# Kernel optimization log

Hardware: AMD Instinct MI355X
Metric: run time of the kernel (lower is better)

## Reference

```python
import jax, jax.numpy as jnp
import numpy as np

B, H, W = 64, 512, 512
T = 100           # num_thresholds
R = 8             # defect regions per image (max label id)
BLOCK = 128       # defect regions are 128x128 blocks on a 4x4 grid
SAT = 1.0         # saturation_threshold (relative)


def setup_inputs() -> dict:
    key = jax.random.key(0)
    k1, _ = jax.random.split(key)
    preds = jax.random.uniform(k1, (B, H, W), dtype=jnp.float32)
    thresholds = jnp.linspace(0.0, 1.0, T).astype(jnp.float32)
    # Build a labeled GT mask: R disjoint 128x128 block regions per image,
    # labels 1..R (0 = background). This plays the role of measure.label(target).
    rng = np.random.default_rng(0)
    labels = np.zeros((B, H, W), dtype=np.int32)
    gb = H // BLOCK           # 4 blocks per side -> 16 candidate blocks
    nblocks = gb * gb
    for b in range(B):
        chosen = rng.permutation(nblocks)[:R]
        for rid, blk in enumerate(chosen, start=1):
            r, c = divmod(int(blk), gb)
            labels[b, r * BLOCK:(r + 1) * BLOCK, c * BLOCK:(c + 1) * BLOCK] = rid
    return {"preds": preds, "thresholds": thresholds, "labels": jnp.asarray(labels)}


def reference(preds, thresholds, labels):
    # preds: (B,H,W) float32 in [0,1); thresholds: (T,) sorted; labels: (B,H,W) int32, 0=bg.
    Bn, Hn, Wn = preds.shape
    Tn = thresholds.shape[0]
    flat_s = preds.reshape(-1)
    flat_l = labels.reshape(-1)
    # bucket[p] = number of thresholds <= score[p]; pixel passes thr[t] iff bucket > t.
    bucket = jnp.searchsorted(thresholds, flat_s, side='right')  # int in [0, T]
    # ---- background FP / TN per threshold (exact counts via histogram) ----
    bg = (flat_l == 0).astype(jnp.int32)
    bg_hist = jax.ops.segment_sum(bg, bucket, num_segments=Tn + 1)  # (T+1,)
    bg_total = bg_hist.sum()
    fp = (bg_total - jnp.cumsum(bg_hist)[:Tn]).astype(jnp.float32)  # fp[t] = #bg with score>=thr[t]
    tn = bg_total.astype(jnp.float32) - fp
    # ---- per-region TP per threshold (segmented histogram) ----
    bidx = jnp.repeat(jnp.arange(Bn), Hn * Wn)
    seg = bidx * R + (flat_l - 1)              # region id in [0, B*R)
    comb = seg * (Tn + 1) + bucket
    NSEG = Bn * R * (Tn + 1)
    comb = jnp.where(flat_l > 0, comb, NSEG)   # dump bg pixels in overflow slot
    hist = jax.ops.segment_sum(jnp.ones_like(bucket, dtype=jnp.int32), comb,
                               num_segments=NSEG + 1)[:NSEG].reshape(Bn, R, Tn + 1)
    area = hist.sum(-1)                                       # (B,R) defect areas
    tp = (area[..., None] - jnp.cumsum(hist, -1)[..., :Tn]).astype(jnp.float32)  # (B,R,T)
    sat = jnp.maximum(area.astype(jnp.float32) * SAT, 1.0)    # relative saturation
    valid = (area > 0).astype(jnp.float32)                    # guard empty regions
    spro = jnp.minimum(tp / sat[..., None], 1.0) * valid[..., None]
    spro_sum = spro.sum((0, 1))                               # (T,)
    n_def = jnp.maximum(valid.sum(), 1.0)
    mean_spro = spro_sum / n_def
    # ---- AUC over FPR (max_fpr = 1.0) ----
    denom = fp + tn
    fpr = jnp.where(denom > 0, fp / jnp.maximum(denom, 1.0), 0.0)
    order = jnp.argsort(fpr)
    x = fpr[order]
    y = mean_spro[order]
    auc = jnp.sum((x[1:] - x[:-1]) * (y[1:] + y[:-1]) * 0.5)  # trapezoid rule
    return auc
```

## Files before the change

### kernel.cpp

```cpp
#include <hip/hip_runtime.h>

#define B_N 64
#define H_N 512
#define W_N 512
#define T_N 100
#define TB  101
#define R_N 8
#define NLAB 9
#define CHUNKS 32
#define PIX_PER_IMG (H_N * W_N)
#define CPIX (PIX_PER_IMG / CHUNKS)

__global__ __launch_bounds__(256, 8) void hist_kernel(
    const float* __restrict__ preds, const int* __restrict__ labels,
    const float* __restrict__ thr,
    int* __restrict__ region_hist,
    int* __restrict__ bg_hist)
{
    __shared__ float s_thr[T_N];
    __shared__ int whist[4][NLAB * TB];

    const int tid  = threadIdx.x;
    const int wave = tid >> 6;

    for (int i = tid; i < 4 * NLAB * TB; i += 256) ((int*)whist)[i] = 0;
    if (tid < T_N) s_thr[tid] = thr[tid];
    __syncthreads();

    const int img   = blockIdx.x >> 5;
    const int chunk = blockIdx.x & (CHUNKS - 1);
    const long base = (long)img * PIX_PER_IMG + (long)chunk * CPIX;
    const float4* p4 = (const float4*)(preds + base);
    const int4*   l4 = (const int4*)(labels + base);
    int* __restrict__ myh = whist[wave];

#pragma unroll
    for (int g = 0; g < 2; ++g) {
        float4 pv[4];
        int4   lv[4];
#pragma unroll
        for (int u = 0; u < 4; ++u) {
            pv[u] = p4[(g * 4 + u) * 256 + tid];
            lv[u] = l4[(g * 4 + u) * 256 + tid];
        }
#pragma unroll
        for (int u = 0; u < 4; ++u) {
            float ps[4] = {pv[u].x, pv[u].y, pv[u].z, pv[u].w};
            int   ls[4] = {lv[u].x, lv[u].y, lv[u].z, lv[u].w};
#pragma unroll
            for (int j = 0; j < 4; ++j) {
                float s = ps[j];
                int k = (int)(s * (float)(T_N - 1)) + 1;
                k = max(0, min(T_N, k));
                while (k < T_N && s_thr[k] <= s) ++k;
                while (k > 0 && s_thr[k - 1] > s) --k;
                atomicAdd(&myh[ls[j] * TB + k], 1);
            }
        }
    }
    __syncthreads();

    for (int i = tid; i < NLAB * TB; i += 256) {
        int v = whist[0][i] + whist[1][i] + whist[2][i] + whist[3][i];
        if (v) {
            int lab = i / TB;
            int t   = i - lab * TB;
            if (lab == 0)
                atomicAdd(&bg_hist[img * TB + t], v);
            else
                atomicAdd(&region_hist[(img * R_N + (lab - 1)) * TB + t], v);
        }
    }
}

__global__ __launch_bounds__(128) void region_final_kernel(
    const int* __restrict__ region_hist,
    const int* __restrict__ bg_hist,
    float* __restrict__ spro_sum,
    int* __restrict__ n_def,
    int* __restrict__ bgh_total,
    int* __restrict__ done_ctr,
    float* __restrict__ out)
{
    __shared__ float spro_sh[R_N][T_N];
    __shared__ int validc[R_N];
    __shared__ int s_ticket;
    const int img = blockIdx.x;
    const int tid = threadIdx.x;

    if (tid < TB) atomicAdd(&bgh_total[tid], bg_hist[img * TB + tid]);

    if (tid < R_N) {
        const int* h = &region_hist[(img * R_N + tid) * TB];
        int area = 0;
        for (int t = 0; t < TB; ++t) area += h[t];
        float sat   = fmaxf((float)area, 1.0f);
        float valid = (area > 0) ? 1.0f : 0.0f;
        int csum = 0;
        for (int t = 0; t < T_N; ++t) {
            csum += h[t];
            float tp = (float)(area - csum);
            spro_sh[tid][t] = fminf(tp / sat, 1.0f) * valid;
        }
        validc[tid] = (area > 0) ? 1 : 0;
    }
    __syncthreads();

    if (tid < T_N) {
        float s = 0.0f;
        for (int r = 0; r < R_N; ++r) s += spro_sh[r][tid];
        atomicAdd(&spro_sum[tid], s);
    }
    if (tid == 0) {
        int v = 0;
        for (int r = 0; r < R_N; ++r) v += validc[r];
        atomicAdd(n_def, v);
    }

    __threadfence();
    if (tid == 0)
        s_ticket = __hip_atomic_fetch_add(done_ctr, 1, __ATOMIC_ACQ_REL,
                                          __HIP_MEMORY_SCOPE_AGENT);
    __syncthreads();
    if (s_ticket != B_N - 1) return;

    __shared__ int    bgh[TB];
    __shared__ float  s_spro[T_N];
    __shared__ float  fpr_sh[T_N];
    __shared__ float  ms_sh[T_N];
    __shared__ int    order[T_N];
    __shared__ double contrib[T_N];
    __shared__ int    s_nd;

    if (tid < TB)
        bgh[tid] = __hip_atomic_load(&bgh_total[tid], __ATOMIC_RELAXED,
                                     __HIP_MEMORY_SCOPE_AGENT);
    if (tid < T_N)
        s_spro[tid] = __hip_atomic_load(&spro_sum[tid], __ATOMIC_RELAXED,
                                        __HIP_MEMORY_SCOPE_AGENT);
    if (tid == 0)
        s_nd = __hip_atomic_load(n_def, __ATOMIC_RELAXED,
                                 __HIP_MEMORY_SCOPE_AGENT);
    __syncthreads();

    if (tid < T_N) {
        int fp_i = 0;
        for (int k = tid + 1; k < TB; ++k) fp_i += bgh[k];
        int tot = fp_i;
        for (int k = 0; k <= tid; ++k) tot += bgh[k];
        float bgt = (float)tot;
        float fp  = (float)fp_i;
        fpr_sh[tid] = (bgt > 0.0f) ? fp / fmaxf(bgt, 1.0f) : 0.0f;
        float nd = fmaxf((float)s_nd, 1.0f);
        ms_sh[tid] = s_spro[tid] / nd;
    }
    __syncthreads();

    if (tid < T_N) {
        float v = fpr_sh[tid];
        int r = 0;
        for (int j = 0; j < T_N; ++j) {
            float u = fpr_sh[j];
            r += (u < v) | ((u == v) & (j < tid));
        }
        order[r] = tid;
    }
    __syncthreads();

    if (tid < T_N - 1) {
        int o0 = order[tid], o1 = order[tid + 1];
        double x0 = fpr_sh[o0], x1 = fpr_sh[o1];
        double y0 = ms_sh[o0],  y1 = ms_sh[o1];
        contrib[tid] = (x1 - x0) * (y0 + y1) * 0.5;
    } else if (tid < T_N) {
        contrib[tid] = 0.0;
    }
    __syncthreads();

    if (tid == 0) {
        double s = 0.0;
        for (int i = 0; i < T_N - 1; ++i) s += contrib[i];
        out[0] = (float)s;
    }
}

extern "C" void kernel_launch(void* const* d_in, const int* in_sizes, int n_in,
                              void* d_out, int out_size, void* d_ws, size_t ws_size,
                              hipStream_t stream) {
    const float* preds  = (const float*)d_in[0];
    const float* thr    = (const float*)d_in[1];
    const int*   labels = (const int*)d_in[2];
    float* out = (float*)d_out;

    int*   region_hist = (int*)d_ws;
    int*   bg_hist     = region_hist + B_N * R_N * TB;
    int*   bgh_total   = bg_hist + B_N * TB;
    float* spro_sum    = (float*)(bgh_total + TB);
    int*   n_def       = (int*)(spro_sum + T_N);
    int*   done_ctr    = n_def + 1;

    size_t zbytes = sizeof(int) * (size_t)(B_N * R_N * TB + B_N * TB + TB)
                  + sizeof(float) * T_N + 2 * sizeof(int);
    hipMemsetAsync(d_ws, 0, zbytes, stream);

    hist_kernel<<<B_N * CHUNKS, 256, 0, stream>>>(preds, labels, thr,
                                                  region_hist, bg_hist);
    region_final_kernel<<<B_N, 128, 0, stream>>>(region_hist, bg_hist, spro_sum,
                                                 n_def, bgh_total, done_ctr, out);
}
```

Baseline: 172.5 us.

## Fuse histogram and finalize kernels; use LUT for threshold bucket lookup

Merges the per-region finalize and AUC stages into the histogram kernel using per-image and global completion counters, so the last chunk block of each image computes its sPRO and the last image block computes the AUC. This drops one kernel launch. It also replaces the linear threshold search with a 256-cell shared-memory lookup table plus a bounds check, falling back to the old search only when the check fails. Shared memory is reused through a union, and the extra fences and atomics add a serialized tail at the end.

New measurement: 542.9 us. 3.15x slower.

```diff
diff --git a/kernel.cpp b/kernel.cpp
--- a/kernel.cpp
+++ b/kernel.cpp
@@ -10,21 +10,59 @@
 #define CHUNKS 32
 #define PIX_PER_IMG (H_N * W_N)
 #define CPIX (PIX_PER_IMG / CHUNKS)
-
-__global__ __launch_bounds__(256, 8) void hist_kernel(
+#define NCELL 256
+
+struct LutE { float tlo, thrb, thi; int klo; };
+
+union TailU {
+    int whist[4][NLAB * TB];
+    struct {
+        double contrib[T_N];
+        int    rh[R_N * TB];
+        float  spro[R_N][T_N];
+        int    validc[R_N];
+        int    bgh[TB];
+        float  fpr[T_N];
+        float  ms[T_N];
+        int    order[T_N];
+        int    nd;
+    } t;
+};
+
+__global__ __launch_bounds__(256, 8) void fused_kernel(
     const float* __restrict__ preds, const int* __restrict__ labels,
     const float* __restrict__ thr,
     int* __restrict__ region_hist,
-    int* __restrict__ bg_hist)
+    int* __restrict__ bg_hist,
+    float* __restrict__ spro_sum,
+    int* __restrict__ n_def,
+    int* __restrict__ img_ctr,
+    int* __restrict__ done_ctr,
+    float* __restrict__ out)
 {
     __shared__ float s_thr[T_N];
-    __shared__ int whist[4][NLAB * TB];
+    __shared__ __align__(16) LutE lut[NCELL];
+    __shared__ TailU u;
+    __shared__ int s_tick;
 
     const int tid  = threadIdx.x;
     const int wave = tid >> 6;
 
-    for (int i = tid; i < 4 * NLAB * TB; i += 256) ((int*)whist)[i] = 0;
     if (tid < T_N) s_thr[tid] = thr[tid];
+    for (int i = tid; i < 4 * NLAB * TB; i += 256) ((int*)u.whist)[i] = 0;
+    __syncthreads();
+
+    if (tid < NCELL) {
+        float lo = (float)tid * (1.0f / (float)NCELL);
+        int a = 0, b = T_N;
+        while (a < b) { int m = (a + b) >> 1; if (s_thr[m] <= lo) a = m + 1; else b = m; }
+        LutE e;
+        e.tlo  = (a > 0)        ? s_thr[a - 1] : -2.0f;
+        e.thrb = (a < T_N)      ? s_thr[a]     :  2.0f;
+        e.thi  = (a + 1 < T_N)  ? s_thr[a + 1] :  2.0f;
+        e.klo  = a;
+        lut[tid] = e;
+    }
     __syncthreads();
 
     const int img   = blockIdx.x >> 5;
@@ -32,28 +70,36 @@
     const long base = (long)img * PIX_PER_IMG + (long)chunk * CPIX;
     const float4* p4 = (const float4*)(preds + base);
     const int4*   l4 = (const int4*)(labels + base);
-    int* __restrict__ myh = whist[wave];
+    int* __restrict__ myh = u.whist[wave];
 
 #pragma unroll
     for (int g = 0; g < 2; ++g) {
         float4 pv[4];
         int4   lv[4];
 #pragma unroll
-        for (int u = 0; u < 4; ++u) {
-            pv[u] = p4[(g * 4 + u) * 256 + tid];
-            lv[u] = l4[(g * 4 + u) * 256 + tid];
-        }
-#pragma unroll
-        for (int u = 0; u < 4; ++u) {
-            float ps[4] = {pv[u].x, pv[u].y, pv[u].z, pv[u].w};
-            int   ls[4] = {lv[u].x, lv[u].y, lv[u].z, lv[u].w};
+        for (int q = 0; q < 4; ++q) {
+            pv[q] = p4[(g * 4 + q) * 256 + tid];
+            lv[q] = l4[(g * 4 + q) * 256 + tid];
+        }
+#pragma unroll
+        for (int q = 0; q < 4; ++q) {
+            float ps[4] = {pv[q].x, pv[q].y, pv[q].z, pv[q].w};
+            int   ls[4] = {lv[q].x, lv[q].y, lv[q].z, lv[q].w};
 #pragma unroll
             for (int j = 0; j < 4; ++j) {
                 float s = ps[j];
-                int k = (int)(s * (float)(T_N - 1)) + 1;
-                k = max(0, min(T_N, k));
-                while (k < T_N && s_thr[k] <= s) ++k;
-                while (k > 0 && s_thr[k - 1] > s) --k;
+                int c = (int)(s * (float)NCELL);
+                c = max(0, min(NCELL - 1, c));
+                LutE e = lut[c];
+                int ge = (s >= e.thrb) ? 1 : 0;
+                int k = e.klo + ge;
+                float lowv  = ge ? e.thrb : e.tlo;
+                float highv = ge ? e.thi  : e.thrb;
+                if (__builtin_expect(!(lowv <= s && s < highv), 0)) {
+                    k = max(0, min(T_N, k));
+                    while (k < T_N && s_thr[k] <= s) ++k;
+                    while (k > 0 && s_thr[k - 1] > s) --k;
+                }
                 atomicAdd(&myh[ls[j] * TB + k], 1);
             }
         }
@@ -61,7 +107,7 @@
     __syncthreads();
 
     for (int i = tid; i < NLAB * TB; i += 256) {
-        int v = whist[0][i] + whist[1][i] + whist[2][i] + whist[3][i];
+        int v = u.whist[0][i] + u.whist[1][i] + u.whist[2][i] + u.whist[3][i];
         if (v) {
             int lab = i / TB;
             int t   = i - lab * TB;
@@ -71,27 +117,22 @@
                 atomicAdd(&region_hist[(img * R_N + (lab - 1)) * TB + t], v);
         }
     }
-}
-
-__global__ __launch_bounds__(128) void region_final_kernel(
-    const int* __restrict__ region_hist,
-    const int* __restrict__ bg_hist,
-    float* __restrict__ spro_sum,
-    int* __restrict__ n_def,
-    int* __restrict__ bgh_total,
-    int* __restrict__ done_ctr,
-    float* __restrict__ out)
-{
-    __shared__ float spro_sh[R_N][T_N];
-    __shared__ int validc[R_N];
-    __shared__ int s_ticket;
-    const int img = blockIdx.x;
-    const int tid = threadIdx.x;
-
-    if (tid < TB) atomicAdd(&bgh_total[tid], bg_hist[img * TB + tid]);
+
+    __threadfence();
+    __syncthreads();
+    if (tid == 0)
+        s_tick = __hip_atomic_fetch_add(&img_ctr[img], 1, __ATOMIC_ACQ_REL,
+                                        __HIP_MEMORY_SCOPE_AGENT);
+    __syncthreads();
+    if (s_tick != CHUNKS - 1) return;
+
+    for (int i = tid; i < R_N * TB; i += 256)
+        u.t.rh[i] = __hip_atomic_load(&region_hist[img * R_N * TB + i],
+                                      __ATOMIC_RELAXED, __HIP_MEMORY_SCOPE_AGENT);
+    __syncthreads();
 
     if (tid < R_N) {
-        const int* h = &region_hist[(img * R_N + tid) * TB];
+        const int* h = &u.t.rh[tid * TB];
         int area = 0;
         for (int t = 0; t < TB; ++t) area += h[t];
         float sat   = fmaxf((float)area, 1.0f);
@@ -99,88 +140,82 @@
         int csum = 0;
         for (int t = 0; t < T_N; ++t) {
             csum += h[t];
-            float tp = (float)(area - csum);
-            spro_sh[tid][t] = fminf(tp / sat, 1.0f) * valid;
-        }
-        validc[tid] = (area > 0) ? 1 : 0;
+            u.t.spro[tid][t] = fminf((float)(area - csum) / sat, 1.0f) * valid;
+        }
+        u.t.validc[tid] = (area > 0) ? 1 : 0;
     }
     __syncthreads();
 
     if (tid < T_N) {
-        float s = 0.0f;
-        for (int r = 0; r < R_N; ++r) s += spro_sh[r][tid];
-        atomicAdd(&spro_sum[tid], s);
+        float ssum = 0.0f;
+        for (int r = 0; r < R_N; ++r) ssum += u.t.spro[r][tid];
+        atomicAdd(&spro_sum[tid], ssum);
     }
     if (tid == 0) {
         int v = 0;
-        for (int r = 0; r < R_N; ++r) v += validc[r];
+        for (int r = 0; r < R_N; ++r) v += u.t.validc[r];
         atomicAdd(n_def, v);
     }
 
     __threadfence();
+    __syncthreads();
     if (tid == 0)
-        s_ticket = __hip_atomic_fetch_add(done_ctr, 1, __ATOMIC_ACQ_REL,
-                                          __HIP_MEMORY_SCOPE_AGENT);
-    __syncthreads();
-    if (s_ticket != B_N - 1) return;
-
-    __shared__ int    bgh[TB];
-    __shared__ float  s_spro[T_N];
-    __shared__ float  fpr_sh[T_N];
-    __shared__ float  ms_sh[T_N];
-    __shared__ int    order[T_N];
-    __shared__ double contrib[T_N];
-    __shared__ int    s_nd;
-
-    if (tid < TB)
-        bgh[tid] = __hip_atomic_load(&bgh_total[tid], __ATOMIC_RELAXED,
-                                     __HIP_MEMORY_SCOPE_AGENT);
+        s_tick = __hip_atomic_fetch_add(done_ctr, 1, __ATOMIC_ACQ_REL,
+                                        __HIP_MEMORY_SCOPE_AGENT);
+    __syncthreads();
+    if (s_tick != B_N - 1) return;
+
+    if (tid < TB) {
+        int ssum = 0;
+        for (int b = 0; b < B_N; ++b)
+            ssum += __hip_atomic_load(&bg_hist[b * TB + tid],
+                                      __ATOMIC_RELAXED, __HIP_MEMORY_SCOPE_AGENT);
+        u.t.bgh[tid] = ssum;
+    }
     if (tid < T_N)
-        s_spro[tid] = __hip_atomic_load(&spro_sum[tid], __ATOMIC_RELAXED,
-                                        __HIP_MEMORY_SCOPE_AGENT);
+        u.t.ms[tid] = __hip_atomic_load(&spro_sum[tid],
+                                        __ATOMIC_RELAXED, __HIP_MEMORY_SCOPE_AGENT);
     if (tid == 0)
-        s_nd = __hip_atomic_load(n_def, __ATOMIC_RELAXED,
-                                 __HIP_MEMORY_SCOPE_AGENT);
+        u.t.nd = __hip_atomic_load(n_def, __ATOMIC_RELAXED,
+                                   __HIP_MEMORY_SCOPE_AGENT);
     __syncthreads();
 
     if (tid < T_N) {
         int fp_i = 0;
-        for (int k = tid + 1; k < TB; ++k) fp_i += bgh[k];
+        for (int k = tid + 1; k < TB; ++k) fp_i += u.t.bgh[k];
         int tot = fp_i;
-        for (int k = 0; k <= tid; ++k) tot += bgh[k];
+        for (int k = 0; k <= tid; ++k) tot += u.t.bgh[k];
         float bgt = (float)tot;
-        float fp  = (float)fp_i;
-        fpr_sh[tid] = (bgt > 0.0f) ? fp / fmaxf(bgt, 1.0f) : 0.0f;
-        float nd = fmaxf((float)s_nd, 1.0f);
-        ms_sh[tid] = s_spro[tid] / nd;
+        u.t.fpr[tid] = (bgt > 0.0f) ? (float)fp_i / fmaxf(bgt, 1.0f) : 0.0f;
+        u.t.ms[tid]  = u.t.ms[tid] / fmaxf((float)u.t.nd, 1.0f);
     }
     __syncthreads();
 
     if (tid < T_N) {
-        float v = fpr_sh[tid];
+        float v = u.t.fpr[tid];
         int r = 0;
         for (int j = 0; j < T_N; ++j) {
-            float u = fpr_sh[j];
-            r += (u < v) | ((u == v) & (j < tid));
-        }
-        order[r] = tid;
+            float w = u.t.fpr[j];
+            r += (w < v) | ((w == v) & (j < tid));
+        }
+        u.t.order[r] = tid;
     }
     __syncthreads();
 
     if (tid < T_N - 1) {
-        int o0 = order[tid], o1 = order[tid + 1];
-        double x0 = fpr_sh[o0], x1 = fpr_sh[o1];
-        double y0 = ms_sh[o0],  y1 = ms_sh[o1];
-        contrib[tid] = (x1 - x0) * (y0 + y1) * 0.5;
+        int o0 = u.t.order[tid], o1 = u.t.order[tid + 1];
+        double x0 = u.t.fpr[o0], x1 = u.t.fpr[o1];
+        double y0 = u.t.ms[o0],  y1 = u.t.ms[o1];
+        u.t.contrib[tid] = (x1 - x0) * (y0 + y1) * 0.5;
     } else if (tid < T_N) {
-        contrib[tid] = 0.0;
+        u.t.contrib[tid] = 0.0;
     }
     __syncthreads();
 
     if (tid == 0) {
-        double s = 0.0;
-        for (int i = 0; i < T_N - 1; ++i) s += contrib[i];
-        out[0] = (float)s;
+        double ssum = 0.0;
+        for (int i = 0; i < T_N - 1; ++i) ssum += u.t.contrib[i];
+        out[0] = (float)ssum;
     }
 }
 
@@ -194,17 +229,16 @@
 
     int*   region_hist = (int*)d_ws;
     int*   bg_hist     = region_hist + B_N * R_N * TB;
-    int*   bgh_total   = bg_hist + B_N * TB;
-    float* spro_sum    = (float*)(bgh_total + TB);
+    float* spro_sum    = (float*)(bg_hist + B_N * TB);
     int*   n_def       = (int*)(spro_sum + T_N);
-    int*   done_ctr    = n_def + 1;
-
-    size_t zbytes = sizeof(int) * (size_t)(B_N * R_N * TB + B_N * TB + TB)
-                  + sizeof(float) * T_N + 2 * sizeof(int);
+    int*   img_ctr     = n_def + 1;
+    int*   done_ctr    = img_ctr + B_N;
+
+    size_t zbytes = sizeof(int) *
+        (size_t)(B_N * R_N * TB + B_N * TB + T_N + 1 + B_N + 1);
     hipMemsetAsync(d_ws, 0, zbytes, stream);
 
-    hist_kernel<<<B_N * CHUNKS, 256, 0, stream>>>(preds, labels, thr,
-                                                  region_hist, bg_hist);
-    region_final_kernel<<<B_N, 128, 0, stream>>>(region_hist, bg_hist, spro_sum,
-                                                 n_def, bgh_total, done_ctr, out);
+    fused_kernel<<<B_N * CHUNKS, 256, 0, stream>>>(
+        preds, labels, thr, region_hist, bg_hist,
+        spro_sum, n_def, img_ctr, done_ctr, out);
 }
```
